# Kernel tuning notes

Hardware: AMD Instinct MI355X
Metric: run time of the kernel (lower is better)

Reference implementation:

```python
import jax, jax.numpy as jnp
import numpy as np

BATCH = 32
ROW_DIM = 8192
COL_DIM = 8192
N_BLOCKS = 512
ROW_BS = ROW_DIM // N_BLOCKS  # 16
COL_BS = COL_DIM // N_BLOCKS  # 16


def setup_inputs() -> dict:
    key = jax.random.key(0)
    k1, k2 = jax.random.split(key)
    x = jax.random.normal(k1, (BATCH, COL_DIM), dtype=jnp.float32)
    # xavier-uniform-ish init scale for blocks [n_blocks, p, q]
    limit = np.sqrt(6.0 / (ROW_BS + COL_BS))
    blocks = jax.random.uniform(k2, (N_BLOCKS, ROW_BS, COL_BS), dtype=jnp.float32,
                                minval=-limit, maxval=limit)
    return {"x": x, "blocks": blocks}


def reference(x, blocks):
    b = x.shape[0]
    n, p, q = blocks.shape
    x_blocks = x.reshape(b, n, q)  # [B, n, q]
    # circulant index pattern: block (i, j) uses blocks[(i - j) % n]
    idx = (jnp.arange(n)[:, None] - jnp.arange(n)[None, :]) % n  # [n, n]
    blocks_shifted = blocks[idx]  # [n, n, p, q] -- the gather-expand intermediate
    y_blocks = jnp.einsum('mnpq,bnq->bmp', blocks_shifted, x_blocks)  # [B, n, p]
    return y_blocks.reshape(b, n * p)
```

## Files before the change

kernel.cpp:

```cpp
#include <hip/hip_runtime.h>
#include <hip/hip_bf16.h>

#define DIM 8192
#define KSPLIT 16
#define PARTIAL_ELEMS (32 * DIM)

typedef __bf16 bf16x8 __attribute__((ext_vector_type(8)));
typedef __bf16 bf16x2 __attribute__((ext_vector_type(2)));
typedef float f32x4 __attribute__((ext_vector_type(4)));
typedef float f32x2 __attribute__((ext_vector_type(2)));

__device__ __forceinline__ uint2 cvt_f4(const float4 v) {
  bf16x2 lo = __builtin_convertvector((f32x2){v.x, v.y}, bf16x2);
  bf16x2 hi = __builtin_convertvector((f32x2){v.z, v.w}, bf16x2);
  uint2 r;
  r.x = __builtin_bit_cast(unsigned, lo);
  r.y = __builtin_bit_cast(unsigned, hi);
  return r;
}

__global__ __launch_bounds__(512, 4)
void bcl_mfma_kernel(const float* __restrict__ X,
                     const float* __restrict__ Blk,
                     float* __restrict__ Ws) {
  __shared__ __align__(16) unsigned short Xl[16384];
  __shared__ __align__(16) unsigned short Wl[47 * 256];

  const int tid = threadIdx.x;
  const int mc  = blockIdx.x & 31;
  const int kc  = blockIdx.x >> 5;
  const int kbase = kc * 512;

  #pragma unroll
  for (int it = 0; it < 8; ++it) {
    const int L  = (tid + it * 512) << 2;
    const int j4 = L & 7;
    const int p  = (L >> 3) & 15;
    const int kh = (L >> 7) & 3;
    const int b0 = (L >> 9) & 1;
    const int s  = (L >> 10) & 15;
    const int batch = b0 * 16 + p;
    const int kg = kbase + s * 32 + (kh >> 1) * 16 + (kh & 1) * 8 + j4;
    const float4 v = *reinterpret_cast<const float4*>(X + batch * DIM + kg);
    *reinterpret_cast<uint2*>(&Xl[L]) = cvt_f4(v);
  }

  const int dbase = (mc * 16 - kc * 32 - 31) & 511;
  for (int i = tid; i < 47 * 64; i += 512) {
    const int w  = i >> 6;
    const int r  = (i & 63) << 2;
    const int qh = r >> 7;
    const int p  = (r >> 3) & 15;
    const int j4 = r & 7;
    const int d  = (dbase + w) & 511;
    const float4 v = *reinterpret_cast<const float4*>(Blk + d * 256 + p * 16 + qh * 8 + j4);
    *reinterpret_cast<uint2*>(&Wl[w * 256 + r]) = cvt_f4(v);
  }

  __syncthreads();

  const int lane = tid & 63;
  const int wid  = tid >> 6;

  const unsigned short* Xb = &Xl[lane << 3];
  const unsigned short* Wb = &Wl[(((lane >> 5) ^ 1) << 8) + (((lane >> 4) & 1) << 7) + ((lane & 15) << 3)];

  f32x4 acc[2][2];
  #pragma unroll
  for (int t = 0; t < 2; ++t)
    #pragma unroll
    for (int b = 0; b < 2; ++b)
      acc[t][b] = (f32x4){0.f, 0.f, 0.f, 0.f};

  #pragma unroll 4
  for (int s = 0; s < 16; ++s) {
    const bf16x8 x0 = *reinterpret_cast<const bf16x8*>(Xb + (s << 10));
    const bf16x8 x1 = *reinterpret_cast<const bf16x8*>(Xb + (s << 10) + 512);
    #pragma unroll
    for (int t = 0; t < 2; ++t) {
      const int mt = (wid << 1) + t;
      const bf16x8 wf = *reinterpret_cast<const bf16x8*>(Wb + ((mt + 30 - 2 * s) << 8));
      acc[t][0] = __builtin_amdgcn_mfma_f32_16x16x32_bf16(x0, wf, acc[t][0], 0, 0, 0);
      acc[t][1] = __builtin_amdgcn_mfma_f32_16x16x32_bf16(x1, wf, acc[t][1], 0, 0, 0);
    }
  }

  float* base = Ws + (size_t)kc * PARTIAL_ELEMS + mc * 256;
  #pragma unroll
  for (int t = 0; t < 2; ++t) {
    const int col = ((wid << 1) + t) * 16 + (lane & 15);
    #pragma unroll
    for (int b0 = 0; b0 < 2; ++b0) {
      const int brow = b0 * 16 + ((lane >> 4) << 2);
      #pragma unroll
      for (int r = 0; r < 4; ++r)
        base[(brow + r) * DIM + col] = acc[t][b0][r];
    }
  }
}

__global__ __launch_bounds__(256)
void bcl_reduce_kernel(const float2* __restrict__ Ws, float2* __restrict__ Out) {
  const int f = blockIdx.x * 256 + threadIdx.x;
  float2 a = Ws[f];
  #pragma unroll
  for (int kc = 1; kc < KSPLIT; ++kc) {
    const float2 v = Ws[kc * (PARTIAL_ELEMS / 2) + f];
    a.x += v.x; a.y += v.y;
  }
  Out[f] = a;
}

extern "C" void kernel_launch(void* const* d_in, const int* in_sizes, int n_in,
                              void* d_out, int out_size, void* d_ws, size_t ws_size,
                              hipStream_t stream) {
  const float* X   = (const float*)d_in[0];
  const float* Blk = (const float*)d_in[1];
  float* Ws  = (float*)d_ws;
  float* Out = (float*)d_out;
  bcl_mfma_kernel<<<dim3(512), dim3(512), 0, stream>>>(X, Blk, Ws);
  bcl_reduce_kernel<<<dim3(PARTIAL_ELEMS / 2 / 256), dim3(256), 0, stream>>>(
      (const float2*)Ws, (float2*)Out);
}
```

Baseline: 70.73 us.

## Pre-pack bf16 operands, load via global_load_lds, atomically reduce split-K outputs

Adds a prep kernel that converts X and the blocks to bf16 in the MFMA-friendly layout once and zeroes the output. The main kernel then copies the packed tiles straight into LDS with global_load_lds instead of converting per block. The separate split-K reduction kernel and its partial-sum workspace are replaced by float atomicAdd into the output. This removes the large partial-buffer write and re-read and the redundant per-block conversion, at the cost of atomic contention across the 16 K-splits and non-deterministic summation order.

```diff
diff --git a/kernel.cpp b/kernel.cpp
--- a/kernel.cpp
+++ b/kernel.cpp
@@ -2,8 +2,6 @@
 #include <hip/hip_bf16.h>
 
 #define DIM 8192
-#define KSPLIT 16
-#define PARTIAL_ELEMS (32 * DIM)
 
 typedef __bf16 bf16x8 __attribute__((ext_vector_type(8)));
 typedef __bf16 bf16x2 __attribute__((ext_vector_type(2)));
@@ -19,48 +17,82 @@
   return r;
 }
 
+#define GL2LDS(gp, lp)                                                        \
+  __builtin_amdgcn_global_load_lds(                                           \
+      (const __attribute__((address_space(1))) void*)(gp),                    \
+      (__attribute__((address_space(3))) void*)(lp), 16, 0, 0)
+
+__global__ __launch_bounds__(256)
+void bcl_prep_kernel(const float* __restrict__ X, const float* __restrict__ Blk,
+                     unsigned short* __restrict__ Xp, unsigned short* __restrict__ Wp,
+                     float4* __restrict__ Out) {
+  const int T = blockIdx.x * 256 + threadIdx.x;
+  if (T < 32768) {
+    const int c  = T;
+    const int p  = c & 15;
+    const int kh = (c >> 4) & 3;
+    const int b0 = (c >> 6) & 1;
+    const int s  = (c >> 7) & 15;
+    const int kc = c >> 11;
+    const float* src = X + (b0 * 16 + p) * DIM + kc * 512 + s * 32 +
+                       ((kh >> 1) << 4) + ((kh & 1) << 3);
+    const float4 v0 = reinterpret_cast<const float4*>(src)[0];
+    const float4 v1 = reinterpret_cast<const float4*>(src)[1];
+    const uint2 a = cvt_f4(v0), b = cvt_f4(v1);
+    uint4 o; o.x = a.x; o.y = a.y; o.z = b.x; o.w = b.y;
+    *reinterpret_cast<uint4*>(Xp + c * 8) = o;
+  } else if (T < 49152) {
+    const int b  = T - 32768;
+    const int d  = b >> 5;
+    const int q5 = b & 31;
+    const int p  = q5 & 15;
+    const int qh = q5 >> 4;
+    const float* src = Blk + d * 256 + p * 16 + qh * 8;
+    const float4 v0 = reinterpret_cast<const float4*>(src)[0];
+    const float4 v1 = reinterpret_cast<const float4*>(src)[1];
+    const uint2 a = cvt_f4(v0), bb = cvt_f4(v1);
+    uint4 o; o.x = a.x; o.y = a.y; o.z = bb.x; o.w = bb.y;
+    *reinterpret_cast<uint4*>(Wp + b * 8) = o;
+  } else {
+    const int z = T - 49152;
+    const float4 zero = {0.f, 0.f, 0.f, 0.f};
+    #pragma unroll
+    for (int i = 0; i < 4; ++i) Out[z * 4 + i] = zero;
+  }
+}
+
 __global__ __launch_bounds__(512, 4)
-void bcl_mfma_kernel(const float* __restrict__ X,
-                     const float* __restrict__ Blk,
-                     float* __restrict__ Ws) {
+void bcl_mfma_kernel(const unsigned short* __restrict__ Xp,
+                     const unsigned short* __restrict__ Wp,
+                     float* __restrict__ Out) {
   __shared__ __align__(16) unsigned short Xl[16384];
-  __shared__ __align__(16) unsigned short Wl[47 * 256];
+  __shared__ __align__(16) unsigned short Wl[48 * 256];
 
-  const int tid = threadIdx.x;
-  const int mc  = blockIdx.x & 31;
-  const int kc  = blockIdx.x >> 5;
-  const int kbase = kc * 512;
+  const int tid  = threadIdx.x;
+  const int lane = tid & 63;
+  const int wid  = tid >> 6;
+  const int mc   = blockIdx.x & 31;
+  const int kc   = blockIdx.x >> 5;
 
+  const char* xsrc = reinterpret_cast<const char*>(Xp + kc * 16384);
   #pragma unroll
-  for (int it = 0; it < 8; ++it) {
-    const int L  = (tid + it * 512) << 2;
-    const int j4 = L & 7;
-    const int p  = (L >> 3) & 15;
-    const int kh = (L >> 7) & 3;
-    const int b0 = (L >> 9) & 1;
-    const int s  = (L >> 10) & 15;
-    const int batch = b0 * 16 + p;
-    const int kg = kbase + s * 32 + (kh >> 1) * 16 + (kh & 1) * 8 + j4;
-    const float4 v = *reinterpret_cast<const float4*>(X + batch * DIM + kg);
-    *reinterpret_cast<uint2*>(&Xl[L]) = cvt_f4(v);
+  for (int ro = 0; ro < 4; ++ro) {
+    const int lb = ro * 8192 + wid * 1024;
+    GL2LDS(xsrc + lb + lane * 16, reinterpret_cast<char*>(Xl) + lb);
   }
 
   const int dbase = (mc * 16 - kc * 32 - 31) & 511;
-  for (int i = tid; i < 47 * 64; i += 512) {
-    const int w  = i >> 6;
-    const int r  = (i & 63) << 2;
-    const int qh = r >> 7;
-    const int p  = (r >> 3) & 15;
-    const int j4 = r & 7;
+  const char* wsrc = reinterpret_cast<const char*>(Wp);
+  #pragma unroll
+  for (int ro = 0; ro < 3; ++ro) {
+    const int lb = ro * 8192 + wid * 1024;
+    const int B  = lb + lane * 16;
+    const int w  = B >> 9;
     const int d  = (dbase + w) & 511;
-    const float4 v = *reinterpret_cast<const float4*>(Blk + d * 256 + p * 16 + qh * 8 + j4);
-    *reinterpret_cast<uint2*>(&Wl[w * 256 + r]) = cvt_f4(v);
+    GL2LDS(wsrc + d * 512 + (B & 511), reinterpret_cast<char*>(Wl) + lb);
   }
 
   __syncthreads();
-
-  const int lane = tid & 63;
-  const int wid  = tid >> 6;
 
   const unsigned short* Xb = &Xl[lane << 3];
   const unsigned short* Wb = &Wl[(((lane >> 5) ^ 1) << 8) + (((lane >> 4) & 1) << 7) + ((lane & 15) << 3)];
@@ -85,7 +117,7 @@
     }
   }
 
-  float* base = Ws + (size_t)kc * PARTIAL_ELEMS + mc * 256;
+  float* outp = Out + mc * 256;
   #pragma unroll
   for (int t = 0; t < 2; ++t) {
     const int col = ((wid << 1) + t) * 16 + (lane & 15);
@@ -94,21 +126,9 @@
       const int brow = b0 * 16 + ((lane >> 4) << 2);
       #pragma unroll
       for (int r = 0; r < 4; ++r)
-        base[(brow + r) * DIM + col] = acc[t][b0][r];
+        atomicAdd(outp + (brow + r) * DIM + col, acc[t][b0][r]);
     }
   }
-}
-
-__global__ __launch_bounds__(256)
-void bcl_reduce_kernel(const float2* __restrict__ Ws, float2* __restrict__ Out) {
-  const int f = blockIdx.x * 256 + threadIdx.x;
-  float2 a = Ws[f];
-  #pragma unroll
-  for (int kc = 1; kc < KSPLIT; ++kc) {
-    const float2 v = Ws[kc * (PARTIAL_ELEMS / 2) + f];
-    a.x += v.x; a.y += v.y;
-  }
-  Out[f] = a;
 }
 
 extern "C" void kernel_launch(void* const* d_in, const int* in_sizes, int n_in,
@@ -116,9 +136,10 @@
                               hipStream_t stream) {
   const float* X   = (const float*)d_in[0];
   const float* Blk = (const float*)d_in[1];
-  float* Ws  = (float*)d_ws;
+  unsigned short* Xp = (unsigned short*)d_ws;
+  unsigned short* Wp = Xp + 262144;
   float* Out = (float*)d_out;
-  bcl_mfma_kernel<<<dim3(512), dim3(512), 0, stream>>>(X, Blk, Ws);
-  bcl_reduce_kernel<<<dim3(PARTIAL_ELEMS / 2 / 256), dim3(256), 0, stream>>>(
-      (const float2*)Ws, (float2*)Out);
+
+  bcl_prep_kernel<<<dim3(256), dim3(256), 0, stream>>>(X, Blk, Xp, Wp, (float4*)Out);
+  bcl_mfma_kernel<<<dim3(512), dim3(512), 0, stream>>>(Xp, Wp, Out);
 }
```

After: 71.95 us. About the same (+1.7%).

## Fuse split-K reduction into MFMA kernel using flag-gated atomic adds

Applied to the files above, without the earlier changes.

Removes the separate reduce kernel and the 16-slice partial-sum workspace. The first K-chunk block for each output column tile writes its result directly to the output and then publishes a release flag. The other K-chunk blocks spin on that flag, then add their results into the output with float atomics. This cuts the large partial-buffer write and read traffic and one kernel launch, in exchange for contended L2 atomics and a spin-wait dependency between blocks. The flag is set to a magic value and never cleared, so on repeated calls the later blocks may add before the first block has stored its result, which risks wrong output.

```diff
diff --git a/kernel.cpp b/kernel.cpp
--- a/kernel.cpp
+++ b/kernel.cpp
@@ -2,8 +2,7 @@
 #include <hip/hip_bf16.h>
 
 #define DIM 8192
-#define KSPLIT 16
-#define PARTIAL_ELEMS (32 * DIM)
+#define MAGIC 0x13579BDFu
 
 typedef __bf16 bf16x8 __attribute__((ext_vector_type(8)));
 typedef __bf16 bf16x2 __attribute__((ext_vector_type(2)));
@@ -20,9 +19,10 @@
 }
 
 __global__ __launch_bounds__(512, 4)
-void bcl_mfma_kernel(const float* __restrict__ X,
-                     const float* __restrict__ Blk,
-                     float* __restrict__ Ws) {
+void bcl_fused_kernel(const float* __restrict__ X,
+                      const float* __restrict__ Blk,
+                      float* __restrict__ Out,
+                      unsigned* __restrict__ Flag) {
   __shared__ __align__(16) unsigned short Xl[16384];
   __shared__ __align__(16) unsigned short Wl[47 * 256];
 
@@ -85,30 +85,41 @@
     }
   }
 
-  float* base = Ws + (size_t)kc * PARTIAL_ELEMS + mc * 256;
-  #pragma unroll
-  for (int t = 0; t < 2; ++t) {
-    const int col = ((wid << 1) + t) * 16 + (lane & 15);
+  float* outp = Out + mc * 256;
+  if (kc == 0) {
     #pragma unroll
-    for (int b0 = 0; b0 < 2; ++b0) {
-      const int brow = b0 * 16 + ((lane >> 4) << 2);
+    for (int t = 0; t < 2; ++t) {
+      const int col = ((wid << 1) + t) * 16 + (lane & 15);
       #pragma unroll
-      for (int r = 0; r < 4; ++r)
-        base[(brow + r) * DIM + col] = acc[t][b0][r];
+      for (int b0 = 0; b0 < 2; ++b0) {
+        const int brow = b0 * 16 + ((lane >> 4) << 2);
+        #pragma unroll
+        for (int r = 0; r < 4; ++r)
+          outp[(brow + r) * DIM + col] = acc[t][b0][r];
+      }
+    }
+    __threadfence();
+    __syncthreads();
+    if (tid == 0)
+      __hip_atomic_store(&Flag[mc], MAGIC, __ATOMIC_RELEASE, __HIP_MEMORY_SCOPE_AGENT);
+  } else {
+    if (tid == 0) {
+      while (__hip_atomic_load(&Flag[mc], __ATOMIC_ACQUIRE, __HIP_MEMORY_SCOPE_AGENT) != MAGIC)
+        __builtin_amdgcn_s_sleep(2);
+    }
+    __syncthreads();
+    #pragma unroll
+    for (int t = 0; t < 2; ++t) {
+      const int col = ((wid << 1) + t) * 16 + (lane & 15);
+      #pragma unroll
+      for (int b0 = 0; b0 < 2; ++b0) {
+        const int brow = b0 * 16 + ((lane >> 4) << 2);
+        #pragma unroll
+        for (int r = 0; r < 4; ++r)
+          atomicAdd(outp + (brow + r) * DIM + col, acc[t][b0][r]);
+      }
     }
   }
-}
-
-__global__ __launch_bounds__(256)
-void bcl_reduce_kernel(const float2* __restrict__ Ws, float2* __restrict__ Out) {
-  const int f = blockIdx.x * 256 + threadIdx.x;
-  float2 a = Ws[f];
-  #pragma unroll
-  for (int kc = 1; kc < KSPLIT; ++kc) {
-    const float2 v = Ws[kc * (PARTIAL_ELEMS / 2) + f];
-    a.x += v.x; a.y += v.y;
-  }
-  Out[f] = a;
 }
 
 extern "C" void kernel_launch(void* const* d_in, const int* in_sizes, int n_in,
@@ -116,9 +127,8 @@
                               hipStream_t stream) {
   const float* X   = (const float*)d_in[0];
   const float* Blk = (const float*)d_in[1];
-  float* Ws  = (float*)d_ws;
   float* Out = (float*)d_out;
-  bcl_mfma_kernel<<<dim3(512), dim3(512), 0, stream>>>(X, Blk, Ws);
-  bcl_reduce_kernel<<<dim3(PARTIAL_ELEMS / 2 / 256), dim3(256), 0, stream>>>(
-      (const float2*)Ws, (float2*)Out);
+  unsigned* Flag = (unsigned*)d_ws;
+
+  bcl_fused_kernel<<<dim3(512), dim3(512), 0, stream>>>(X, Blk, Out, Flag);
 }
```

Result: slower. 111.6 us (+57.7%).
